# Performance work log

Hardware: AMD Instinct MI355X
Metric: run time of the kernel (lower is better)

Reference implementation:

```python
import jax, jax.numpy as jnp
import numpy as np

STEEPNESS = 10.0
EPS = 1e-12

def _l2norm(x):
    return x / jnp.sqrt(jnp.sum(x * x, axis=-1, keepdims=True) + EPS)

def setup_inputs() -> dict:
    key = jax.random.key(0)
    k1, k2, k3 = jax.random.split(key, 3)
    B, D, C = 65536, 512, 1024
    return {
        "query": jax.random.normal(k1, (B, D), dtype=jnp.float32),
        "key_mem": jax.random.normal(k2, (C, D), dtype=jnp.float32),
        "val_mem": jax.random.normal(k3, (C, C), dtype=jnp.float32),
    }

def reference(query, key_mem, val_mem):
    # F.normalize(query_vectors, dim=-1)
    q = _l2norm(query)                      # (B, D)
    # cosine_similarity_multi(q, key_mem, rep='real'):
    # F.linear(F.normalize(a), F.normalize(b)) -> (B, C)
    k = _l2norm(key_mem)                    # (C, D)
    sim = jnp.einsum('bd,cd->bc', q, k)     # (B, C)
    # softabs sharpening: sigmoid(s*(x-0.5)) + sigmoid(s*(-x-0.5))
    s = STEEPNESS
    sharp = jax.nn.sigmoid(s * sim - 0.5 * s) + jax.nn.sigmoid(-s * sim - 0.5 * s)
    # normalize_weightings
    w = sharp / jnp.sum(sharp, axis=1, keepdims=True)
    # weighted value readout
    out = jnp.matmul(w, val_mem)            # (B, C)
    return out
```

## Files before the change

kernel.cpp:

```cpp
#include <hip/hip_runtime.h>
#include <hip/hip_bf16.h>

typedef __attribute__((ext_vector_type(8))) short bf16x8;
typedef __attribute__((ext_vector_type(8))) unsigned short ushort8;
typedef __attribute__((ext_vector_type(4))) float f32x4;
typedef unsigned int u32;

#define D_DIM 512
#define C_DIM 1024
#define B_DIM 65536

__device__ __forceinline__ unsigned short f2bf(float x) {
  u32 u = __float_as_uint(x);
  u32 r = (u + 0x7fffu + ((u >> 16) & 1u)) >> 16;
  return (unsigned short)r;
}

__device__ __forceinline__ void async16(const void* g, void* l) {
  __builtin_amdgcn_global_load_lds(
      (const __attribute__((address_space(1))) u32*)g,
      (__attribute__((address_space(3))) u32*)l, 16, 0, 0);
}

__device__ __forceinline__ float sharpf(float x) {
  float t = __expf(10.f * x - 5.f);
  float u = 22026.4658f * t * t;
  float num = u + 2.f * t + 1.f;
  float den = u + 22027.4658f * t + 1.f;
  return num * __builtin_amdgcn_rcpf(den);
}

__global__ __launch_bounds__(256) void rownorm_kernel(
    const float* __restrict__ src, unsigned short* __restrict__ dst) {
  int row = blockIdx.x * 4 + (threadIdx.x >> 6);
  int lane = threadIdx.x & 63;
  const float* s = src + (size_t)row * D_DIM + lane * 8;
  float4 v0 = *(const float4*)s;
  float4 v1 = *(const float4*)(s + 4);
  float ss = v0.x * v0.x + v0.y * v0.y + v0.z * v0.z + v0.w * v0.w +
             v1.x * v1.x + v1.y * v1.y + v1.z * v1.z + v1.w * v1.w;
#pragma unroll
  for (int m = 32; m >= 1; m >>= 1) ss += __shfl_xor(ss, m);
  float rinv = rsqrtf(ss + 1e-12f);
  float tv[8] = {v0.x, v0.y, v0.z, v0.w, v1.x, v1.y, v1.z, v1.w};
  ushort8 o;
#pragma unroll
  for (int i = 0; i < 8; ++i) o[i] = f2bf(tv[i] * rinv);
  *(ushort8*)(dst + (size_t)row * D_DIM + lane * 8) = o;
}

__global__ __launch_bounds__(256) void valT_kernel(
    const float* __restrict__ val, unsigned short* __restrict__ vbT) {
  __shared__ float tile[32][33];
  int bx = blockIdx.x & 31;
  int by = blockIdx.x >> 5;
  int t = threadIdx.x;
  int r = t >> 5, c = t & 31;
#pragma unroll
  for (int i = 0; i < 4; ++i)
    tile[r + i * 8][c] = val[(size_t)(by * 32 + r + i * 8) * C_DIM + bx * 32 + c];
  __syncthreads();
#pragma unroll
  for (int i = 0; i < 4; ++i)
    vbT[(size_t)(bx * 32 + r + i * 8) * C_DIM + by * 32 + c] = f2bf(tile[c][r + i * 8]);
}

__global__ __launch_bounds__(256) void rsum_reduce_kernel(
    const float* __restrict__ part, float* __restrict__ rsum) {
  int i = blockIdx.x * 256 + threadIdx.x;
  rsum[i] = (part[i] + part[i + B_DIM]) +
            (part[i + 2 * B_DIM] + part[i + 3 * B_DIM]);
}

template <int K, bool SHARP>
__global__ __launch_bounds__(512, 2) void gemm256_kernel(
    const unsigned short* __restrict__ A, const unsigned short* __restrict__ Bm,
    unsigned short* __restrict__ wout, float* __restrict__ rsum,
    float* __restrict__ fout) {
  __shared__ unsigned short smem[65536];
  const int NKT = K / 64;
  const int bid = blockIdx.x;
  const int wg = (bid & 7) * 128 + (bid >> 3);
  const int m0 = (wg >> 2) * 256;
  const int n0 = (wg & 3) * 256;
  const int t = threadIdx.x;
  const int lane = t & 63;
  const int wv = t >> 6;
  const int wr = wv >> 2;
  const int wc = wv & 3;
  const int lo = lane & 15, hi = lane >> 4;
  const int swu = (lo & 7) << 3;

  const int s_ridx = t >> 3;
  const int s_c = (t & 7) * 8;
  auto stage = [&](int T) {
    const int d = (T & 1) * 32768;
#pragma unroll
    for (int k = 0; k < 4; ++k) {
      int r = (s_ridx < 32) ? (k * 32 + s_ridx) : (96 + k * 32 + s_ridx);
      int cl = s_c ^ ((r & 7) << 3);
      size_t go = (size_t)T * 64 + cl;
      async16(A + (size_t)(m0 + r) * K + go, &smem[d + r * 64 + s_c]);
      async16(Bm + (size_t)(n0 + r) * K + go, &smem[d + 16384 + r * 64 + s_c]);
    }
  };

  f32x4 acc[8][4];
#pragma unroll
  for (int i = 0; i < 8; ++i)
#pragma unroll
    for (int j = 0; j < 4; ++j) acc[i][j] = (f32x4){0.f, 0.f, 0.f, 0.f};

  stage(0);

#pragma unroll 1
  for (int T = 0; T < NKT; ++T) {
    asm volatile("s_waitcnt vmcnt(0)" ::: "memory");
    __builtin_amdgcn_s_barrier();
    if (T + 1 < NKT) stage(T + 1);
    const int d = (T & 1) * 32768;
    bf16x8 bfr[4][2];
    {
      bf16x8 af[2][2];
#pragma unroll
      for (int mi = 0; mi < 2; ++mi)
#pragma unroll
        for (int ks = 0; ks < 2; ++ks) {
          int r = wr * 128 + mi * 16 + lo;
          af[mi][ks] = *(const bf16x8*)&smem[d + r * 64 + ((ks * 32 + hi * 8) ^ swu)];
        }
#pragma unroll
      for (int nf = 0; nf < 4; ++nf)
#pragma unroll
        for (int ks = 0; ks < 2; ++ks) {
          int r = wc * 64 + nf * 16 + lo;
          bfr[nf][ks] =
              *(const bf16x8*)&smem[d + 16384 + r * 64 + ((ks * 32 + hi * 8) ^ swu)];
        }
      __builtin_amdgcn_s_setprio(1);
#pragma unroll
      for (int mi = 0; mi < 2; ++mi)
#pragma unroll
        for (int nf = 0; nf < 4; ++nf)
#pragma unroll
          for (int ks = 0; ks < 2; ++ks)
            acc[mi][nf] = __builtin_amdgcn_mfma_f32_16x16x32_bf16(
                af[mi][ks], bfr[nf][ks], acc[mi][nf], 0, 0, 0);
      __builtin_amdgcn_s_setprio(0);
    }
#pragma unroll
    for (int p = 1; p < 4; ++p) {
      bf16x8 af[2][2];
#pragma unroll
      for (int mi = 0; mi < 2; ++mi)
#pragma unroll
        for (int ks = 0; ks < 2; ++ks) {
          int r = wr * 128 + (p * 2 + mi) * 16 + lo;
          af[mi][ks] = *(const bf16x8*)&smem[d + r * 64 + ((ks * 32 + hi * 8) ^ swu)];
        }
      __builtin_amdgcn_s_setprio(1);
#pragma unroll
      for (int mi = 0; mi < 2; ++mi)
#pragma unroll
        for (int nf = 0; nf < 4; ++nf)
#pragma unroll
          for (int ks = 0; ks < 2; ++ks)
            acc[p * 2 + mi][nf] = __builtin_amdgcn_mfma_f32_16x16x32_bf16(
                af[mi][ks], bfr[nf][ks], acc[p * 2 + mi][nf], 0, 0, 0);
      __builtin_amdgcn_s_setprio(0);
    }
  }
  __syncthreads();

  if (SHARP) {
    float rs[8][4];
#pragma unroll
    for (int i = 0; i < 8; ++i)
#pragma unroll
      for (int j = 0; j < 4; ++j) rs[i][j] = 0.f;
    unsigned short* ep = smem;
#pragma unroll
    for (int mf = 0; mf < 8; ++mf)
#pragma unroll
      for (int nf = 0; nf < 4; ++nf)
#pragma unroll
        for (int j = 0; j < 4; ++j) {
          float s = sharpf(acc[mf][nf][j]);
          rs[mf][j] += s;
          int rl = wr * 128 + mf * 16 + (hi << 2) + j;
          int cl = (wc * 64 + nf * 16 + lo) ^ (((rl >> 2) & 3) << 4);
          ep[rl * 256 + cl] = f2bf(s);
        }
#pragma unroll
    for (int mf = 0; mf < 8; ++mf)
#pragma unroll
      for (int j = 0; j < 4; ++j) {
        float v = rs[mf][j];
        v += __shfl_xor(v, 1);
        v += __shfl_xor(v, 2);
        v += __shfl_xor(v, 4);
        v += __shfl_xor(v, 8);
        rs[mf][j] = v;
      }
    __syncthreads();
#pragma unroll
    for (int pass = 0; pass < 16; ++pass) {
      int idx = pass * 4096 + t * 8;
      int row = idx >> 8, col = idx & 255;
      int phys = row * 256 + (col ^ (((row >> 2) & 3) << 4));
      *(ushort8*)&wout[(size_t)(m0 + row) * C_DIM + n0 + col] =
          *(const ushort8*)&ep[phys];
    }
    __syncthreads();
    float* rbuf = (float*)smem;
    if (lo == 0) {
#pragma unroll
      for (int mf = 0; mf < 8; ++mf)
#pragma unroll
        for (int j = 0; j < 4; ++j)
          rbuf[wc * 256 + wr * 128 + mf * 16 + (hi << 2) + j] = rs[mf][j];
    }
    __syncthreads();
    if (t < 256) {
      float v = (rbuf[t] + rbuf[256 + t]) + (rbuf[512 + t] + rbuf[768 + t]);
      rsum[(size_t)(wg & 3) * B_DIM + m0 + t] = v;
    }
  } else {
    float rinv[8][4];
#pragma unroll
    for (int mf = 0; mf < 8; ++mf) {
      float4 r4 = *(const float4*)&rsum[m0 + wr * 128 + mf * 16 + (hi << 2)];
      rinv[mf][0] = __builtin_amdgcn_rcpf(r4.x);
      rinv[mf][1] = __builtin_amdgcn_rcpf(r4.y);
      rinv[mf][2] = __builtin_amdgcn_rcpf(r4.z);
      rinv[mf][3] = __builtin_amdgcn_rcpf(r4.w);
    }
#pragma unroll
    for (int mf = 0; mf < 8; ++mf)
#pragma unroll
      for (int nf = 0; nf < 4; ++nf)
#pragma unroll
        for (int j = 0; j < 4; ++j)
          fout[(size_t)(m0 + wr * 128 + mf * 16 + (hi << 2) + j) * C_DIM +
               n0 + wc * 64 + nf * 16 + lo] = acc[mf][nf][j] * rinv[mf][j];
  }
}

extern "C" void kernel_launch(void* const* d_in, const int* in_sizes, int n_in,
                              void* d_out, int out_size, void* d_ws, size_t ws_size,
                              hipStream_t stream) {
  const float* query = (const float*)d_in[0];
  const float* key = (const float*)d_in[1];
  const float* val = (const float*)d_in[2];
  float* out = (float*)d_out;
  const int B = in_sizes[0] / D_DIM;

  char* ws = (char*)d_ws;
  unsigned short* kb = (unsigned short*)(ws);
  unsigned short* vbT = (unsigned short*)(ws + (1ull << 20));
  float* rsum_part = (float*)(ws + 3ull * (1ull << 20));
  unsigned short* qb = (unsigned short*)(ws + 4ull * (1ull << 20));
  float* rsum = (float*)qb;
  unsigned short* wbf = (unsigned short*)(ws + 68ull * (1ull << 20));

  rownorm_kernel<<<dim3(B / 4), dim3(256), 0, stream>>>(query, qb);
  rownorm_kernel<<<dim3(C_DIM / 4), dim3(256), 0, stream>>>(key, kb);
  valT_kernel<<<dim3(1024), dim3(256), 0, stream>>>(val, vbT);

  dim3 grid((B / 256) * (C_DIM / 256));
  gemm256_kernel<D_DIM, true><<<grid, dim3(512), 0, stream>>>(qb, kb, wbf, rsum_part, nullptr);
  rsum_reduce_kernel<<<dim3(B / 256), dim3(256), 0, stream>>>(rsum_part, rsum);
  gemm256_kernel<C_DIM, false><<<grid, dim3(512), 0, stream>>>(wbf, vbT, nullptr, rsum, out);
}
```

Measured before the change: 339.3 us.

## Switch GEMMs to 128x128 tiles with 4-wave blocks and staged prefetch

Replaces the 256x256-tile, 8-wave GEMM with a 128x128-tile, 4-wave kernel that uses a K-step of 32 and a smaller shared-memory footprint. This allows more blocks per CU. The load pipeline is split into two partial stages issued inside the compute loop, with a partial vmcnt wait, to overlap global loads with MFMA. The row-sum partials grow from 4 to 8 column tiles and now live in the output buffer. The trade-off is lower arithmetic intensity per tile, so more global and L2 traffic for operand reloads.

```diff
diff --git a/kernel.cpp b/kernel.cpp
--- a/kernel.cpp
+++ b/kernel.cpp
@@ -68,131 +68,140 @@
 __global__ __launch_bounds__(256) void rsum_reduce_kernel(
     const float* __restrict__ part, float* __restrict__ rsum) {
   int i = blockIdx.x * 256 + threadIdx.x;
-  rsum[i] = (part[i] + part[i + B_DIM]) +
-            (part[i + 2 * B_DIM] + part[i + 3 * B_DIM]);
+  float v = 0.f;
+#pragma unroll
+  for (int j = 0; j < 8; ++j) v += part[i + (size_t)j * B_DIM];
+  rsum[i] = v;
 }
 
 template <int K, bool SHARP>
-__global__ __launch_bounds__(512, 2) void gemm256_kernel(
+__global__ __launch_bounds__(256, 4) void gemm128_kernel(
     const unsigned short* __restrict__ A, const unsigned short* __restrict__ Bm,
     unsigned short* __restrict__ wout, float* __restrict__ rsum,
     float* __restrict__ fout) {
-  __shared__ unsigned short smem[65536];
-  const int NKT = K / 64;
+  __shared__ unsigned short smem[16384];
+  const int NKT = K / 32;
   const int bid = blockIdx.x;
-  const int wg = (bid & 7) * 128 + (bid >> 3);
-  const int m0 = (wg >> 2) * 256;
-  const int n0 = (wg & 3) * 256;
+  const int wg = (bid & 7) * 512 + (bid >> 3);
+  const int m0 = (wg >> 3) * 128;
+  const int n0 = (wg & 7) * 128;
   const int t = threadIdx.x;
   const int lane = t & 63;
   const int wv = t >> 6;
-  const int wr = wv >> 2;
-  const int wc = wv & 3;
+  const int wr = wv >> 1;
+  const int wc = wv & 1;
   const int lo = lane & 15, hi = lane >> 4;
-  const int swu = (lo & 7) << 3;
-
-  const int s_ridx = t >> 3;
-  const int s_c = (t & 7) * 8;
-  auto stage = [&](int T) {
-    const int d = (T & 1) * 32768;
-#pragma unroll
-    for (int k = 0; k < 4; ++k) {
-      int r = (s_ridx < 32) ? (k * 32 + s_ridx) : (96 + k * 32 + s_ridx);
-      int cl = s_c ^ ((r & 7) << 3);
-      size_t go = (size_t)T * 64 + cl;
-      async16(A + (size_t)(m0 + r) * K + go, &smem[d + r * 64 + s_c]);
-      async16(Bm + (size_t)(n0 + r) * K + go, &smem[d + 16384 + r * 64 + s_c]);
+
+  const int rl4 = t >> 2;
+  const int sc = (t & 3) * 8;
+  auto stage_u0 = [&](int T) {
+    const int d = (T & 1) * 8192;
+    {
+      int r = (rl4 >> 5) * 64 + (rl4 & 31);
+      int cl = sc ^ (((r >> 1) & 3) << 3);
+      async16(A + (size_t)(m0 + r) * K + (size_t)T * 32 + cl,
+              &smem[d + r * 32 + sc]);
+    }
+#pragma unroll
+    for (int i = 0; i < 2; ++i) {
+      int s = i * 256 + t;
+      int r = s >> 2, c = (s & 3) * 8;
+      int cl = c ^ (((r >> 1) & 3) << 3);
+      async16(Bm + (size_t)(n0 + r) * K + (size_t)T * 32 + cl,
+              &smem[d + 4096 + r * 32 + c]);
     }
   };
-
-  f32x4 acc[8][4];
-#pragma unroll
-  for (int i = 0; i < 8; ++i)
+  auto stage_u1 = [&](int T) {
+    const int d = (T & 1) * 8192;
+    int r = (rl4 >> 5) * 64 + 32 + (rl4 & 31);
+    int cl = sc ^ (((r >> 1) & 3) << 3);
+    async16(A + (size_t)(m0 + r) * K + (size_t)T * 32 + cl,
+            &smem[d + r * 32 + sc]);
+  };
+
+  f32x4 acc[4][4];
+#pragma unroll
+  for (int i = 0; i < 4; ++i)
 #pragma unroll
     for (int j = 0; j < 4; ++j) acc[i][j] = (f32x4){0.f, 0.f, 0.f, 0.f};
 
-  stage(0);
+  stage_u0(0); stage_u1(0); stage_u0(1);
 
 #pragma unroll 1
   for (int T = 0; T < NKT; ++T) {
-    asm volatile("s_waitcnt vmcnt(0)" ::: "memory");
+    if (T == NKT - 1) {
+      asm volatile("s_waitcnt vmcnt(0)" ::: "memory");
+    } else {
+      asm volatile("s_waitcnt vmcnt(3)" ::: "memory");
+    }
     __builtin_amdgcn_s_barrier();
-    if (T + 1 < NKT) stage(T + 1);
-    const int d = (T & 1) * 32768;
-    bf16x8 bfr[4][2];
+    const int d = (T & 1) * 8192;
+    bf16x8 bfr[4];
     {
-      bf16x8 af[2][2];
+      bf16x8 af[2];
+#pragma unroll
+      for (int mi = 0; mi < 2; ++mi) {
+        int r = wr * 64 + mi * 16 + lo;
+        af[mi] = *(const bf16x8*)&smem[d + r * 32 + ((hi * 8) ^ (((r >> 1) & 3) << 3))];
+      }
+#pragma unroll
+      for (int nf = 0; nf < 4; ++nf) {
+        int r = wc * 64 + nf * 16 + lo;
+        bfr[nf] =
+            *(const bf16x8*)&smem[d + 4096 + r * 32 + ((hi * 8) ^ (((r >> 1) & 3) << 3))];
+      }
+      if (T + 1 < NKT) stage_u1(T + 1);
+      __builtin_amdgcn_s_setprio(1);
 #pragma unroll
       for (int mi = 0; mi < 2; ++mi)
 #pragma unroll
-        for (int ks = 0; ks < 2; ++ks) {
-          int r = wr * 128 + mi * 16 + lo;
-          af[mi][ks] = *(const bf16x8*)&smem[d + r * 64 + ((ks * 32 + hi * 8) ^ swu)];
-        }
-#pragma unroll
-      for (int nf = 0; nf < 4; ++nf)
-#pragma unroll
-        for (int ks = 0; ks < 2; ++ks) {
-          int r = wc * 64 + nf * 16 + lo;
-          bfr[nf][ks] =
-              *(const bf16x8*)&smem[d + 16384 + r * 64 + ((ks * 32 + hi * 8) ^ swu)];
-        }
+        for (int nf = 0; nf < 4; ++nf)
+          acc[mi][nf] = __builtin_amdgcn_mfma_f32_16x16x32_bf16(
+              af[mi], bfr[nf], acc[mi][nf], 0, 0, 0);
+      __builtin_amdgcn_s_setprio(0);
+    }
+    {
+      bf16x8 af[2];
+#pragma unroll
+      for (int mi = 0; mi < 2; ++mi) {
+        int r = wr * 64 + (2 + mi) * 16 + lo;
+        af[mi] = *(const bf16x8*)&smem[d + r * 32 + ((hi * 8) ^ (((r >> 1) & 3) << 3))];
+      }
+      __builtin_amdgcn_s_barrier();
+      if (T + 2 < NKT) stage_u0(T + 2);
       __builtin_amdgcn_s_setprio(1);
 #pragma unroll
       for (int mi = 0; mi < 2; ++mi)
 #pragma unroll
         for (int nf = 0; nf < 4; ++nf)
-#pragma unroll
-          for (int ks = 0; ks < 2; ++ks)
-            acc[mi][nf] = __builtin_amdgcn_mfma_f32_16x16x32_bf16(
-                af[mi][ks], bfr[nf][ks], acc[mi][nf], 0, 0, 0);
-      __builtin_amdgcn_s_setprio(0);
-    }
-#pragma unroll
-    for (int p = 1; p < 4; ++p) {
-      bf16x8 af[2][2];
-#pragma unroll
-      for (int mi = 0; mi < 2; ++mi)
-#pragma unroll
-        for (int ks = 0; ks < 2; ++ks) {
-          int r = wr * 128 + (p * 2 + mi) * 16 + lo;
-          af[mi][ks] = *(const bf16x8*)&smem[d + r * 64 + ((ks * 32 + hi * 8) ^ swu)];
-        }
-      __builtin_amdgcn_s_setprio(1);
-#pragma unroll
-      for (int mi = 0; mi < 2; ++mi)
-#pragma unroll
-        for (int nf = 0; nf < 4; ++nf)
-#pragma unroll
-          for (int ks = 0; ks < 2; ++ks)
-            acc[p * 2 + mi][nf] = __builtin_amdgcn_mfma_f32_16x16x32_bf16(
-                af[mi][ks], bfr[nf][ks], acc[p * 2 + mi][nf], 0, 0, 0);
+          acc[2 + mi][nf] = __builtin_amdgcn_mfma_f32_16x16x32_bf16(
+              af[mi], bfr[nf], acc[2 + mi][nf], 0, 0, 0);
       __builtin_amdgcn_s_setprio(0);
     }
   }
   __syncthreads();
 
   if (SHARP) {
-    float rs[8][4];
-#pragma unroll
-    for (int i = 0; i < 8; ++i)
+    float rs[4][4];
+#pragma unroll
+    for (int i = 0; i < 4; ++i)
 #pragma unroll
       for (int j = 0; j < 4; ++j) rs[i][j] = 0.f;
     unsigned short* ep = smem;
 #pragma unroll
-    for (int mf = 0; mf < 8; ++mf)
+    for (int mf = 0; mf < 4; ++mf)
 #pragma unroll
       for (int nf = 0; nf < 4; ++nf)
 #pragma unroll
         for (int j = 0; j < 4; ++j) {
           float s = sharpf(acc[mf][nf][j]);
           rs[mf][j] += s;
-          int rl = wr * 128 + mf * 16 + (hi << 2) + j;
+          int rl = wr * 64 + mf * 16 + (hi << 2) + j;
           int cl = (wc * 64 + nf * 16 + lo) ^ (((rl >> 2) & 3) << 4);
-          ep[rl * 256 + cl] = f2bf(s);
+          ep[rl * 128 + cl] = f2bf(s);
         }
 #pragma unroll
-    for (int mf = 0; mf < 8; ++mf)
+    for (int mf = 0; mf < 4; ++mf)
 #pragma unroll
       for (int j = 0; j < 4; ++j) {
         float v = rs[mf][j];
@@ -204,10 +213,10 @@
       }
     __syncthreads();
 #pragma unroll
-    for (int pass = 0; pass < 16; ++pass) {
-      int idx = pass * 4096 + t * 8;
-      int row = idx >> 8, col = idx & 255;
-      int phys = row * 256 + (col ^ (((row >> 2) & 3) << 4));
+    for (int pass = 0; pass < 8; ++pass) {
+      int idx = pass * 2048 + t * 8;
+      int row = idx >> 7, col = idx & 127;
+      int phys = row * 128 + (col ^ (((row >> 2) & 3) << 4));
       *(ushort8*)&wout[(size_t)(m0 + row) * C_DIM + n0 + col] =
           *(const ushort8*)&ep[phys];
     }
@@ -215,33 +224,32 @@
     float* rbuf = (float*)smem;
     if (lo == 0) {
 #pragma unroll
-      for (int mf = 0; mf < 8; ++mf)
+      for (int mf = 0; mf < 4; ++mf)
 #pragma unroll
         for (int j = 0; j < 4; ++j)
-          rbuf[wc * 256 + wr * 128 + mf * 16 + (hi << 2) + j] = rs[mf][j];
+          rbuf[wc * 128 + wr * 64 + mf * 16 + (hi << 2) + j] = rs[mf][j];
     }
     __syncthreads();
-    if (t < 256) {
-      float v = (rbuf[t] + rbuf[256 + t]) + (rbuf[512 + t] + rbuf[768 + t]);
-      rsum[(size_t)(wg & 3) * B_DIM + m0 + t] = v;
+    if (t < 128) {
+      rsum[(size_t)(wg & 7) * B_DIM + m0 + t] = rbuf[t] + rbuf[128 + t];
     }
   } else {
-    float rinv[8][4];
-#pragma unroll
-    for (int mf = 0; mf < 8; ++mf) {
-      float4 r4 = *(const float4*)&rsum[m0 + wr * 128 + mf * 16 + (hi << 2)];
+    float rinv[4][4];
+#pragma unroll
+    for (int mf = 0; mf < 4; ++mf) {
+      float4 r4 = *(const float4*)&rsum[m0 + wr * 64 + mf * 16 + (hi << 2)];
       rinv[mf][0] = __builtin_amdgcn_rcpf(r4.x);
       rinv[mf][1] = __builtin_amdgcn_rcpf(r4.y);
       rinv[mf][2] = __builtin_amdgcn_rcpf(r4.z);
       rinv[mf][3] = __builtin_amdgcn_rcpf(r4.w);
     }
 #pragma unroll
-    for (int mf = 0; mf < 8; ++mf)
+    for (int mf = 0; mf < 4; ++mf)
 #pragma unroll
       for (int nf = 0; nf < 4; ++nf)
 #pragma unroll
         for (int j = 0; j < 4; ++j)
-          fout[(size_t)(m0 + wr * 128 + mf * 16 + (hi << 2) + j) * C_DIM +
+          fout[(size_t)(m0 + wr * 64 + mf * 16 + (hi << 2) + j) * C_DIM +
                n0 + wc * 64 + nf * 16 + lo] = acc[mf][nf][j] * rinv[mf][j];
   }
 }
@@ -258,17 +266,17 @@
   char* ws = (char*)d_ws;
   unsigned short* kb = (unsigned short*)(ws);
   unsigned short* vbT = (unsigned short*)(ws + (1ull << 20));
-  float* rsum_part = (float*)(ws + 3ull * (1ull << 20));
   unsigned short* qb = (unsigned short*)(ws + 4ull * (1ull << 20));
   float* rsum = (float*)qb;
+  float* rsum_part = (float*)d_out;
   unsigned short* wbf = (unsigned short*)(ws + 68ull * (1ull << 20));
 
   rownorm_kernel<<<dim3(B / 4), dim3(256), 0, stream>>>(query, qb);
   rownorm_kernel<<<dim3(C_DIM / 4), dim3(256), 0, stream>>>(key, kb);
   valT_kernel<<<dim3(1024), dim3(256), 0, stream>>>(val, vbT);
 
-  dim3 grid((B / 256) * (C_DIM / 256));
-  gemm256_kernel<D_DIM, true><<<grid, dim3(512), 0, stream>>>(qb, kb, wbf, rsum_part, nullptr);
+  dim3 grid((B / 128) * (C_DIM / 128));
+  gemm128_kernel<D_DIM, true><<<grid, dim3(256), 0, stream>>>(qb, kb, wbf, rsum_part, nullptr);
   rsum_reduce_kernel<<<dim3(B / 256), dim3(256), 0, stream>>>(rsum_part, rsum);
-  gemm256_kernel<C_DIM, false><<<grid, dim3(512), 0, stream>>>(wbf, vbT, nullptr, rsum, out);
-}
+  gemm128_kernel<C_DIM, false><<<grid, dim3(256), 0, stream>>>(wbf, vbT, nullptr, rsum, out);
+}
```

Measured after the change: 347.9 us. +2.5%, slower.
